# Kernel optimization log

Hardware: AMD Instinct MI355X
Metric: run time of the kernel (lower is better)

The kernel has to match this reference:

```python
import jax, jax.numpy as jnp
import numpy as np

N_ATOMS = 25000
IN_FEATURES = 128
OUT_FEATURES = 128
N_SPECIES = 64


def setup_inputs() -> dict:
    key = jax.random.key(0)
    k1, k2, k3, k4 = jax.random.split(key, 4)
    features = jax.random.normal(k1, (N_ATOMS, IN_FEATURES), dtype=jnp.float32)
    species_idx = jax.random.randint(k2, (N_ATOMS,), 0, N_SPECIES, dtype=jnp.int64)
    # kaiming_uniform_ with a=sqrt(5) on fan_in gives bound = 1/sqrt(fan_in);
    # bias init uses the same bound.
    bound = 1.0 / np.sqrt(IN_FEATURES)
    weight = jax.random.uniform(
        k3, (N_SPECIES, OUT_FEATURES, IN_FEATURES), dtype=jnp.float32,
        minval=-bound, maxval=bound)
    bias = jax.random.uniform(
        k4, (N_SPECIES, OUT_FEATURES), dtype=jnp.float32,
        minval=-bound, maxval=bound)
    return {"features": features, "species_idx": species_idx,
            "weight": weight, "bias": bias}


def reference(features, species_idx, weight, bias):
    # Species-indexed weight gather + per-atom GEMV (batched matmul with q=1).
    # W[idx]: (n_atoms, out_features, in_features)
    W = jnp.take(weight, species_idx, axis=0)
    b = jnp.take(bias, species_idx, axis=0)  # (n_atoms, out_features)
    out = jnp.einsum("ni,noi->no", features, W) + b
    return out
```

## Files before the change

### kernel.cpp

```cpp
#include <hip/hip_runtime.h>

#define NATOMS 25000
#define NSP 64
#define NRANGE 16
#define RSIZE ((NATOMS + NRANGE - 1) / NRANGE)

typedef short bf16x8 __attribute__((ext_vector_type(8)));
typedef float f32x4  __attribute__((ext_vector_type(4)));
typedef unsigned short u16;

__device__ __forceinline__ u16 f2bf(float f) {
  unsigned u = __float_as_uint(f);
  u += 0x7fffu + ((u >> 16) & 1u);
  return (u16)(u >> 16);
}

__global__ __launch_bounds__(256)
void zcl_kernel(const float* __restrict__ feat,
                const int*   __restrict__ sp,
                const float* __restrict__ weight,
                const float* __restrict__ bias,
                float*       __restrict__ out)
{
  __shared__ u16 Ws[128 * 128];
  __shared__ u16 As[16 * 128];
  __shared__ u16 list[((RSIZE + 15) & ~15) + 16];
  __shared__ int nM;

  const int tid = threadIdx.x;
  const int bid = blockIdx.x;
  const int s  = bid >> 4;
  const int r  = bid & (NRANGE - 1);
  const int lo = r * RSIZE;
  const int hi = (lo + RSIZE < NATOMS) ? (lo + RSIZE) : NATOMS;

  if (tid == 0) nM = 0;

  const int wv   = tid >> 6;
  const int lane = tid & 63;
  const int l16  = lane & 15;
  const int kq   = lane >> 4;
  const int o0   = wv * 32 + l16;
  const float bv0 = bias[s * 128 + o0];
  const float bv1 = bias[s * 128 + o0 + 16];

  const float4* wg = (const float4*)(weight + (size_t)s * (128 * 128));
  #pragma unroll
  for (int j = 0; j < 8; ++j) {
    int chunk = j * 256 + tid;
    int row = chunk >> 4;
    int c   = chunk & 15;
    float4 v0 = wg[row * 32 + c * 2];
    float4 v1 = wg[row * 32 + c * 2 + 1];
    union { u16 h[8]; bf16x8 v; } uu;
    uu.h[0] = f2bf(v0.x); uu.h[1] = f2bf(v0.y);
    uu.h[2] = f2bf(v0.z); uu.h[3] = f2bf(v0.w);
    uu.h[4] = f2bf(v1.x); uu.h[5] = f2bf(v1.y);
    uu.h[6] = f2bf(v1.z); uu.h[7] = f2bf(v1.w);
    *(bf16x8*)&Ws[row * 128 + ((c ^ (row & 7)) << 3)] = uu.v;
  }

  __syncthreads();

  for (int a0 = lo; a0 < hi; a0 += 256) {
    int a = a0 + tid;
    bool m = (a < hi) && (sp[a] == s);
    unsigned long long mk = __ballot(m);
    int base = 0;
    if (lane == 0) base = atomicAdd(&nM, __popcll(mk));
    base = __shfl(base, 0);
    if (m) list[base + __popcll(mk & ((1ull << lane) - 1ull))] = (u16)a;
  }
  __syncthreads();

  const int nMatch = nM;
  const int ntile  = (nMatch + 15) >> 4;

  for (int t = 0; t < ntile; ++t) {
    __syncthreads();
    {
      int row = tid >> 4, c = tid & 15;
      int li  = t * 16 + row;
      int atom = list[li < nMatch ? li : 0];
      const float4* xg = (const float4*)(feat + (size_t)atom * 128);
      float4 v0 = xg[c * 2];
      float4 v1 = xg[c * 2 + 1];
      union { u16 h[8]; bf16x8 v; } uu;
      uu.h[0] = f2bf(v0.x); uu.h[1] = f2bf(v0.y);
      uu.h[2] = f2bf(v0.z); uu.h[3] = f2bf(v0.w);
      uu.h[4] = f2bf(v1.x); uu.h[5] = f2bf(v1.y);
      uu.h[6] = f2bf(v1.z); uu.h[7] = f2bf(v1.w);
      *(bf16x8*)&As[row * 128 + ((c ^ (row & 7)) << 3)] = uu.v;
    }
    __syncthreads();

    f32x4 acc0 = {0.f, 0.f, 0.f, 0.f};
    f32x4 acc1 = {0.f, 0.f, 0.f, 0.f};
    const int br0 = wv * 32 + l16;
    const int br1 = br0 + 16;
    #pragma unroll
    for (int ks = 0; ks < 4; ++ks) {
      int slot = ks * 4 + kq;
      bf16x8 av = *(const bf16x8*)&As[l16 * 128 + ((slot ^ (l16 & 7)) << 3)];
      bf16x8 b0 = *(const bf16x8*)&Ws[br0 * 128 + ((slot ^ (br0 & 7)) << 3)];
      bf16x8 b1 = *(const bf16x8*)&Ws[br1 * 128 + ((slot ^ (br1 & 7)) << 3)];
      acc0 = __builtin_amdgcn_mfma_f32_16x16x32_bf16(av, b0, acc0, 0, 0, 0);
      acc1 = __builtin_amdgcn_mfma_f32_16x16x32_bf16(av, b1, acc1, 0, 0, 0);
    }

    #pragma unroll
    for (int q = 0; q < 4; ++q) {
      int li = t * 16 + kq * 4 + q;
      if (li < nMatch) {
        int atom = list[li];
        float* op = out + (size_t)atom * 128 + o0;
        op[0]  = acc0[q] + bv0;
        op[16] = acc1[q] + bv1;
      }
    }
  }
}

extern "C" void kernel_launch(void* const* d_in, const int* in_sizes, int n_in,
                              void* d_out, int out_size, void* d_ws, size_t ws_size,
                              hipStream_t stream) {
  const float* feat   = (const float*)d_in[0];
  const int*   sp     = (const int*)d_in[1];
  const float* weight = (const float*)d_in[2];
  const float* bias   = (const float*)d_in[3];
  float*       out    = (float*)d_out;
  zcl_kernel<<<NSP * NRANGE, 256, 0, stream>>>(feat, sp, weight, bias, out);
}
```

Measured before the change: 18.04 us.

## Pre-convert weights to bf16 and stream them into LDS with prefetched features

A separate kernel now converts all weights to bf16 once. The main kernel copies its species' bf16 weight tile straight from global memory into LDS with global_load_lds, instead of having 16 blocks each reload and convert the fp32 weights. Species indices are loaded into registers before the weight copy, and the next feature tile is prefetched into registers while the current tile runs its MFMAs. Blocks with no matching atoms now exit early. In exchange this adds a second launch and workspace traffic, and the wait before the barrier uses lgkmcnt rather than vmcnt, which may not be enough for the asynchronous LDS load.

```diff
diff --git a/kernel.cpp b/kernel.cpp
--- a/kernel.cpp
+++ b/kernel.cpp
@@ -4,10 +4,13 @@
 #define NSP 64
 #define NRANGE 16
 #define RSIZE ((NATOMS + NRANGE - 1) / NRANGE)
+#define SCAN_IT ((RSIZE + 255) / 256)
 
 typedef short bf16x8 __attribute__((ext_vector_type(8)));
 typedef float f32x4  __attribute__((ext_vector_type(4)));
 typedef unsigned short u16;
+typedef __attribute__((address_space(3))) unsigned int  lds_u32;
+typedef __attribute__((address_space(1))) unsigned int  gbl_u32;
 
 __device__ __forceinline__ u16 f2bf(float f) {
   unsigned u = __float_as_uint(f);
@@ -16,9 +19,22 @@
 }
 
 __global__ __launch_bounds__(256)
+void conv_w_kernel(const float* __restrict__ w, u16* __restrict__ wbf) {
+  int i = (blockIdx.x * 256 + threadIdx.x) * 8;
+  const float4* p = (const float4*)(w + i);
+  float4 v0 = p[0], v1 = p[1];
+  union { u16 h[8]; bf16x8 v; } uu;
+  uu.h[0] = f2bf(v0.x); uu.h[1] = f2bf(v0.y);
+  uu.h[2] = f2bf(v0.z); uu.h[3] = f2bf(v0.w);
+  uu.h[4] = f2bf(v1.x); uu.h[5] = f2bf(v1.y);
+  uu.h[6] = f2bf(v1.z); uu.h[7] = f2bf(v1.w);
+  *(bf16x8*)(wbf + i) = uu.v;
+}
+
+__global__ __launch_bounds__(256)
 void zcl_kernel(const float* __restrict__ feat,
                 const int*   __restrict__ sp,
-                const float* __restrict__ weight,
+                const u16*   __restrict__ wbf,
                 const float* __restrict__ bias,
                 float*       __restrict__ out)
 {
@@ -34,65 +50,76 @@
   const int lo = r * RSIZE;
   const int hi = (lo + RSIZE < NATOMS) ? (lo + RSIZE) : NATOMS;
 
-  if (tid == 0) nM = 0;
-
   const int wv   = tid >> 6;
   const int lane = tid & 63;
   const int l16  = lane & 15;
   const int kq   = lane >> 4;
   const int o0   = wv * 32 + l16;
+
   const float bv0 = bias[s * 128 + o0];
   const float bv1 = bias[s * 128 + o0 + 16];
 
-  const float4* wg = (const float4*)(weight + (size_t)s * (128 * 128));
+  int spv[SCAN_IT];
+  #pragma unroll
+  for (int i = 0; i < SCAN_IT; ++i) {
+    int a = lo + i * 256 + tid;
+    spv[i] = (a < hi) ? sp[a] : -1;
+  }
+
+  const u16* wsrc = wbf + (size_t)s * (128 * 128);
   #pragma unroll
   for (int j = 0; j < 8; ++j) {
-    int chunk = j * 256 + tid;
-    int row = chunk >> 4;
-    int c   = chunk & 15;
-    float4 v0 = wg[row * 32 + c * 2];
-    float4 v1 = wg[row * 32 + c * 2 + 1];
-    union { u16 h[8]; bf16x8 v; } uu;
-    uu.h[0] = f2bf(v0.x); uu.h[1] = f2bf(v0.y);
-    uu.h[2] = f2bf(v0.z); uu.h[3] = f2bf(v0.w);
-    uu.h[4] = f2bf(v1.x); uu.h[5] = f2bf(v1.y);
-    uu.h[6] = f2bf(v1.z); uu.h[7] = f2bf(v1.w);
-    *(bf16x8*)&Ws[row * 128 + ((c ^ (row & 7)) << 3)] = uu.v;
+    int m   = j * 256 + tid;
+    int row = m >> 4;
+    int cs  = m & 15;
+    const u16* src = wsrc + row * 128 + ((cs ^ (row & 7)) << 3);
+    u16* dst = &Ws[(j * 256 + (tid & ~63)) * 8];
+    __builtin_amdgcn_global_load_lds((gbl_u32*)src, (lds_u32*)dst, 16, 0, 0);
   }
 
-  __syncthreads();
+  if (tid == 0) nM = 0;
+  asm volatile("s_waitcnt lgkmcnt(0)" ::: "memory");
+  __builtin_amdgcn_s_barrier();
 
-  for (int a0 = lo; a0 < hi; a0 += 256) {
-    int a = a0 + tid;
-    bool m = (a < hi) && (sp[a] == s);
+  #pragma unroll
+  for (int i = 0; i < SCAN_IT; ++i) {
+    bool m = (spv[i] == s);
     unsigned long long mk = __ballot(m);
     int base = 0;
     if (lane == 0) base = atomicAdd(&nM, __popcll(mk));
     base = __shfl(base, 0);
-    if (m) list[base + __popcll(mk & ((1ull << lane) - 1ull))] = (u16)a;
+    if (m) list[base + __popcll(mk & ((1ull << lane) - 1ull))] = (u16)(lo + i * 256 + tid);
   }
   __syncthreads();
 
   const int nMatch = nM;
   const int ntile  = (nMatch + 15) >> 4;
+  if (ntile == 0) return;
+
+  const int grow = tid >> 4, gc = tid & 15;
+  float4 pv0, pv1;
+  {
+    int li = grow;
+    int atom = list[li < nMatch ? li : 0];
+    const float4* xg = (const float4*)(feat + (size_t)atom * 128);
+    pv0 = xg[gc * 2]; pv1 = xg[gc * 2 + 1];
+  }
 
   for (int t = 0; t < ntile; ++t) {
+    union { u16 h[8]; bf16x8 v; } uu;
+    uu.h[0] = f2bf(pv0.x); uu.h[1] = f2bf(pv0.y);
+    uu.h[2] = f2bf(pv0.z); uu.h[3] = f2bf(pv0.w);
+    uu.h[4] = f2bf(pv1.x); uu.h[5] = f2bf(pv1.y);
+    uu.h[6] = f2bf(pv1.z); uu.h[7] = f2bf(pv1.w);
+    *(bf16x8*)&As[grow * 128 + ((gc ^ (grow & 7)) << 3)] = uu.v;
     __syncthreads();
-    {
-      int row = tid >> 4, c = tid & 15;
-      int li  = t * 16 + row;
+
+    if (t + 1 < ntile) {
+      int li = (t + 1) * 16 + grow;
       int atom = list[li < nMatch ? li : 0];
       const float4* xg = (const float4*)(feat + (size_t)atom * 128);
-      float4 v0 = xg[c * 2];
-      float4 v1 = xg[c * 2 + 1];
-      union { u16 h[8]; bf16x8 v; } uu;
-      uu.h[0] = f2bf(v0.x); uu.h[1] = f2bf(v0.y);
-      uu.h[2] = f2bf(v0.z); uu.h[3] = f2bf(v0.w);
-      uu.h[4] = f2bf(v1.x); uu.h[5] = f2bf(v1.y);
-      uu.h[6] = f2bf(v1.z); uu.h[7] = f2bf(v1.w);
-      *(bf16x8*)&As[row * 128 + ((c ^ (row & 7)) << 3)] = uu.v;
+      pv0 = xg[gc * 2]; pv1 = xg[gc * 2 + 1];
     }
-    __syncthreads();
 
     f32x4 acc0 = {0.f, 0.f, 0.f, 0.f};
     f32x4 acc1 = {0.f, 0.f, 0.f, 0.f};
@@ -118,6 +145,7 @@
         op[16] = acc1[q] + bv1;
       }
     }
+    __syncthreads();
   }
 }
 
@@ -129,5 +157,8 @@
   const float* weight = (const float*)d_in[2];
   const float* bias   = (const float*)d_in[3];
   float*       out    = (float*)d_out;
-  zcl_kernel<<<NSP * NRANGE, 256, 0, stream>>>(feat, sp, weight, bias, out);
+  u16*         wbf    = (u16*)d_ws;
+
+  conv_w_kernel<<<512, 256, 0, stream>>>(weight, wbf);
+  zcl_kernel<<<NSP * NRANGE, 256, 0, stream>>>(feat, sp, wbf, bias, out);
 }
```

Result: slower. 19.83 us (+10.0%).

## Cut atom ranges per species and give each wave its own atom tile with prefetch

Applied to the files above, without the earlier changes.

Blocks per species drop from 16 atom ranges to 4, so each species' weight matrix is loaded and converted to bf16 fewer times. Species indices and weights are loaded into registers up front so the loads overlap the scan. Each wave now handles a whole 16-atom tile across all 128 outputs, reading features straight from global memory into MFMA operands, with register prefetch of its next tile. This removes the shared A staging and the per-tile block barriers, at the cost of more registers and fewer blocks (256) to spread across the GPU.

```diff
diff --git a/kernel.cpp b/kernel.cpp
--- a/kernel.cpp
+++ b/kernel.cpp
@@ -2,8 +2,9 @@
 
 #define NATOMS 25000
 #define NSP 64
-#define NRANGE 16
+#define NRANGE 4
 #define RSIZE ((NATOMS + NRANGE - 1) / NRANGE)
+#define SCAN_IT ((RSIZE + 255) / 256)
 
 typedef short bf16x8 __attribute__((ext_vector_type(8)));
 typedef float f32x4  __attribute__((ext_vector_type(4)));
@@ -23,99 +24,136 @@
                 float*       __restrict__ out)
 {
   __shared__ u16 Ws[128 * 128];
-  __shared__ u16 As[16 * 128];
-  __shared__ u16 list[((RSIZE + 15) & ~15) + 16];
+  __shared__ u16 list[RSIZE];
   __shared__ int nM;
 
   const int tid = threadIdx.x;
   const int bid = blockIdx.x;
-  const int s  = bid >> 4;
-  const int r  = bid & (NRANGE - 1);
+  const int s  = bid >> 2;
+  const int r  = bid & 3;
   const int lo = r * RSIZE;
   const int hi = (lo + RSIZE < NATOMS) ? (lo + RSIZE) : NATOMS;
-
-  if (tid == 0) nM = 0;
 
   const int wv   = tid >> 6;
   const int lane = tid & 63;
   const int l16  = lane & 15;
   const int kq   = lane >> 4;
-  const int o0   = wv * 32 + l16;
-  const float bv0 = bias[s * 128 + o0];
-  const float bv1 = bias[s * 128 + o0 + 16];
+
+  int spv[SCAN_IT];
+  #pragma unroll
+  for (int i = 0; i < SCAN_IT; ++i) {
+    int a = lo + i * 256 + tid;
+    spv[i] = (a < hi) ? sp[a] : -1;
+  }
+
+  float bv[8];
+  #pragma unroll
+  for (int nf = 0; nf < 8; ++nf) bv[nf] = bias[s * 128 + l16 + 16 * nf];
 
   const float4* wg = (const float4*)(weight + (size_t)s * (128 * 128));
+  float4 wv0[8], wv1[8];
   #pragma unroll
   for (int j = 0; j < 8; ++j) {
-    int chunk = j * 256 + tid;
-    int row = chunk >> 4;
-    int c   = chunk & 15;
-    float4 v0 = wg[row * 32 + c * 2];
-    float4 v1 = wg[row * 32 + c * 2 + 1];
+    int m = j * 256 + tid;
+    int row = m >> 4, c = m & 15;
+    wv0[j] = wg[row * 32 + c * 2];
+    wv1[j] = wg[row * 32 + c * 2 + 1];
+  }
+
+  if (tid == 0) nM = 0;
+  asm volatile("s_waitcnt lgkmcnt(0)" ::: "memory");
+  __builtin_amdgcn_s_barrier();
+  __builtin_amdgcn_sched_barrier(0);
+
+  #pragma unroll
+  for (int i = 0; i < SCAN_IT; ++i) {
+    bool m = (spv[i] == s);
+    unsigned long long mk = __ballot(m);
+    int base = 0;
+    if (lane == 0) base = atomicAdd(&nM, __popcll(mk));
+    base = __shfl(base, 0);
+    if (m) list[base + __popcll(mk & ((1ull << lane) - 1ull))] = (u16)(lo + i * 256 + tid);
+  }
+
+  #pragma unroll
+  for (int j = 0; j < 8; ++j) {
+    int m = j * 256 + tid;
+    int row = m >> 4, c = m & 15;
     union { u16 h[8]; bf16x8 v; } uu;
-    uu.h[0] = f2bf(v0.x); uu.h[1] = f2bf(v0.y);
-    uu.h[2] = f2bf(v0.z); uu.h[3] = f2bf(v0.w);
-    uu.h[4] = f2bf(v1.x); uu.h[5] = f2bf(v1.y);
-    uu.h[6] = f2bf(v1.z); uu.h[7] = f2bf(v1.w);
+    uu.h[0] = f2bf(wv0[j].x); uu.h[1] = f2bf(wv0[j].y);
+    uu.h[2] = f2bf(wv0[j].z); uu.h[3] = f2bf(wv0[j].w);
+    uu.h[4] = f2bf(wv1[j].x); uu.h[5] = f2bf(wv1[j].y);
+    uu.h[6] = f2bf(wv1[j].z); uu.h[7] = f2bf(wv1[j].w);
     *(bf16x8*)&Ws[row * 128 + ((c ^ (row & 7)) << 3)] = uu.v;
   }
 
   __syncthreads();
 
-  for (int a0 = lo; a0 < hi; a0 += 256) {
-    int a = a0 + tid;
-    bool m = (a < hi) && (sp[a] == s);
-    unsigned long long mk = __ballot(m);
-    int base = 0;
-    if (lane == 0) base = atomicAdd(&nM, __popcll(mk));
-    base = __shfl(base, 0);
-    if (m) list[base + __popcll(mk & ((1ull << lane) - 1ull))] = (u16)a;
-  }
-  __syncthreads();
-
   const int nMatch = nM;
   const int ntile  = (nMatch + 15) >> 4;
+  if (ntile == 0) return;
 
-  for (int t = 0; t < ntile; ++t) {
-    __syncthreads();
-    {
-      int row = tid >> 4, c = tid & 15;
-      int li  = t * 16 + row;
-      int atom = list[li < nMatch ? li : 0];
-      const float4* xg = (const float4*)(feat + (size_t)atom * 128);
-      float4 v0 = xg[c * 2];
-      float4 v1 = xg[c * 2 + 1];
-      union { u16 h[8]; bf16x8 v; } uu;
-      uu.h[0] = f2bf(v0.x); uu.h[1] = f2bf(v0.y);
-      uu.h[2] = f2bf(v0.z); uu.h[3] = f2bf(v0.w);
-      uu.h[4] = f2bf(v1.x); uu.h[5] = f2bf(v1.y);
-      uu.h[6] = f2bf(v1.z); uu.h[7] = f2bf(v1.w);
-      *(bf16x8*)&As[row * 128 + ((c ^ (row & 7)) << 3)] = uu.v;
-    }
-    __syncthreads();
-
-    f32x4 acc0 = {0.f, 0.f, 0.f, 0.f};
-    f32x4 acc1 = {0.f, 0.f, 0.f, 0.f};
-    const int br0 = wv * 32 + l16;
-    const int br1 = br0 + 16;
+  int t = wv;
+  float4 pf[8];
+  {
+    int li = t * 16 + l16;
+    int atomA = list[li < nMatch ? li : 0];
+    const float4* xg = (const float4*)(feat + (size_t)atomA * 128);
     #pragma unroll
     for (int ks = 0; ks < 4; ++ks) {
-      int slot = ks * 4 + kq;
-      bf16x8 av = *(const bf16x8*)&As[l16 * 128 + ((slot ^ (l16 & 7)) << 3)];
-      bf16x8 b0 = *(const bf16x8*)&Ws[br0 * 128 + ((slot ^ (br0 & 7)) << 3)];
-      bf16x8 b1 = *(const bf16x8*)&Ws[br1 * 128 + ((slot ^ (br1 & 7)) << 3)];
-      acc0 = __builtin_amdgcn_mfma_f32_16x16x32_bf16(av, b0, acc0, 0, 0, 0);
-      acc1 = __builtin_amdgcn_mfma_f32_16x16x32_bf16(av, b1, acc1, 0, 0, 0);
+      pf[2 * ks]     = xg[ks * 8 + kq * 2];
+      pf[2 * ks + 1] = xg[ks * 8 + kq * 2 + 1];
+    }
+  }
+
+  for (; t < ntile; t += 4) {
+    float4 fv[8];
+    #pragma unroll
+    for (int u = 0; u < 8; ++u) fv[u] = pf[u];
+
+    if (t + 4 < ntile) {
+      int li = (t + 4) * 16 + l16;
+      int atomA = list[li < nMatch ? li : 0];
+      const float4* xg = (const float4*)(feat + (size_t)atomA * 128);
+      #pragma unroll
+      for (int ks = 0; ks < 4; ++ks) {
+        pf[2 * ks]     = xg[ks * 8 + kq * 2];
+        pf[2 * ks + 1] = xg[ks * 8 + kq * 2 + 1];
+      }
+    }
+
+    bf16x8 av[4];
+    #pragma unroll
+    for (int ks = 0; ks < 4; ++ks) {
+      union { u16 h[8]; bf16x8 v; } uu;
+      uu.h[0] = f2bf(fv[2 * ks].x);     uu.h[1] = f2bf(fv[2 * ks].y);
+      uu.h[2] = f2bf(fv[2 * ks].z);     uu.h[3] = f2bf(fv[2 * ks].w);
+      uu.h[4] = f2bf(fv[2 * ks + 1].x); uu.h[5] = f2bf(fv[2 * ks + 1].y);
+      uu.h[6] = f2bf(fv[2 * ks + 1].z); uu.h[7] = f2bf(fv[2 * ks + 1].w);
+      av[ks] = uu.v;
+    }
+
+    f32x4 acc[8];
+    #pragma unroll
+    for (int nf = 0; nf < 8; ++nf) acc[nf] = (f32x4){0.f, 0.f, 0.f, 0.f};
+    #pragma unroll
+    for (int ks = 0; ks < 4; ++ks) {
+      int chunk = ((ks * 4 + kq) ^ (l16 & 7)) << 3;
+      #pragma unroll
+      for (int nf = 0; nf < 8; ++nf) {
+        bf16x8 b = *(const bf16x8*)&Ws[(l16 + 16 * nf) * 128 + chunk];
+        acc[nf] = __builtin_amdgcn_mfma_f32_16x16x32_bf16(av[ks], b, acc[nf], 0, 0, 0);
+      }
     }
 
     #pragma unroll
     for (int q = 0; q < 4; ++q) {
-      int li = t * 16 + kq * 4 + q;
-      if (li < nMatch) {
-        int atom = list[li];
-        float* op = out + (size_t)atom * 128 + o0;
-        op[0]  = acc0[q] + bv0;
-        op[16] = acc1[q] + bv1;
+      int li2 = t * 16 + kq * 4 + q;
+      if (li2 < nMatch) {
+        int atom = list[li2];
+        float* op = out + (size_t)atom * 128 + l16;
+        #pragma unroll
+        for (int nf = 0; nf < 8; ++nf) op[16 * nf] = acc[nf][q] + bv[nf];
       }
     }
   }
```

New measurement: 17.16 us. 1.05x faster.
